# Performance work log

Measured on AMD Instinct MI355X. Metric: run time of the kernel, lower is better.

The kernel has to match this reference:

```python
import jax, jax.numpy as jnp
import numpy as np

B, N, IN_DIM, OUT_DIM, HEADS = 8, 1024, 128, 64, 4

def setup_inputs() -> dict:
    key = jax.random.key(0)
    k1, k2, k3, k4 = jax.random.split(key, 4)
    H = jax.random.normal(k1, (B, N, IN_DIM), dtype=jnp.float32)
    A = jax.random.randint(k2, (B, N, N), 0, 2, dtype=jnp.int32)
    W = jax.random.normal(k3, (IN_DIM, OUT_DIM * HEADS), dtype=jnp.float32) * (1.0 / np.sqrt(IN_DIM))
    a = jax.random.normal(k4, (HEADS, 2 * OUT_DIM), dtype=jnp.float32)
    return {"H": H, "A": A, "W": W, "a": a}

def reference(H, A, W, a):
    Bb, Nn, _ = H.shape
    # Linear projection -> [B, H, N, D]
    Ht = (H @ W).reshape(Bb, Nn, HEADS, OUT_DIM).transpose(0, 2, 1, 3)
    # Split attention vector: e[b,h,n,m] = a_src.Ht[n] + a_dst.Ht[m]
    a_src, a_dst = a[:, :OUT_DIM], a[:, OUT_DIM:]
    e_src = jnp.einsum('bhnd,hd->bhn', Ht, a_src)  # [B,H,N]
    e_dst = jnp.einsum('bhmd,hd->bhm', Ht, a_dst)  # [B,H,N]
    e = e_src[:, :, :, None] + e_dst[:, :, None, :]  # [B,H,N,N]
    e = jax.nn.leaky_relu(e, negative_slope=0.2)
    mask = (A[:, None, :, :] == 0)  # [B,1,N,N]
    e = jnp.where(mask, jnp.float32(-1e9), e)
    alpha = jax.nn.softmax(e, axis=-1)
    H_att = jnp.einsum('bhnm,bhmd->bhnd', alpha, Ht)
    H_out = H_att.transpose(0, 2, 1, 3).reshape(Bb, Nn, HEADS * OUT_DIM)
    return jax.nn.elu(H_out)
```

## Files before the change

kernel.cpp:

```cpp
#include <hip/hip_runtime.h>
#include <hip/hip_bf16.h>
#include <cstdint>
#include <cmath>

#define B_   8
#define N_   1024
#define IND  128
#define D_   64
#define H_   4
#define BH_  (B_*H_)

typedef __attribute__((ext_vector_type(8))) short short8;
typedef __attribute__((ext_vector_type(4))) short shortx4;
typedef __attribute__((ext_vector_type(4))) float f32x4;

__device__ inline short f2bf(float f) {
  __hip_bfloat16 h = __float2bfloat16(f);
  return *reinterpret_cast<short*>(&h);
}

__global__ __launch_bounds__(256) void k_proj(
    const float* __restrict__ H, const float* __restrict__ W,
    const float* __restrict__ a, short* __restrict__ HtT,
    float* __restrict__ esrc, float* __restrict__ edst) {
  __shared__ float hrow[4 * IND];
  const int tid = threadIdx.x;
  const int row0 = blockIdx.x * 4;
  const float* src = H + (size_t)row0 * IND;
  hrow[tid]       = src[tid];
  hrow[tid + 256] = src[tid + 256];
  __syncthreads();

  const int w = tid >> 6;
  const int lane = tid & 63;
  float acc0 = 0.f, acc1 = 0.f, acc2 = 0.f, acc3 = 0.f;
  #pragma unroll 4
  for (int k = 0; k < IND; ++k) {
    float wk = W[k * 256 + tid];
    acc0 = fmaf(hrow[k],           wk, acc0);
    acc1 = fmaf(hrow[IND + k],     wk, acc1);
    acc2 = fmaf(hrow[2 * IND + k], wk, acc2);
    acc3 = fmaf(hrow[3 * IND + k], wk, acc3);
  }
  const float asrc = a[w * 2 * D_ + lane];
  const float adst = a[w * 2 * D_ + D_ + lane];
  float accs[4] = {acc0, acc1, acc2, acc3};

  const int b = row0 >> 10;
  const int n = row0 & (N_ - 1);
  shortx4 hv;
  #pragma unroll
  for (int r = 0; r < 4; ++r) hv[r] = f2bf(accs[r]);
  *(shortx4*)(HtT + ((size_t)((b * H_ + w) * D_ + lane)) * N_ + n) = hv;

  #pragma unroll
  for (int r = 0; r < 4; ++r) {
    float es = accs[r] * asrc;
    float ed = accs[r] * adst;
    #pragma unroll
    for (int off = 32; off >= 1; off >>= 1) {
      es += __shfl_xor(es, off);
      ed += __shfl_xor(ed, off);
    }
    if (lane == 0) {
      size_t eo = (size_t)(b * H_ + w) * N_ + n + r;
      esrc[eo] = es;
      edst[eo] = ed;
    }
  }
}

__global__ __launch_bounds__(256) void k_attn(
    const short* __restrict__ HtT, const float* __restrict__ esrc,
    const float* __restrict__ edst, const int* __restrict__ A,
    float* __restrict__ out) {
  __shared__ float accL[4][16][68];
  __shared__ float MSl[2][4][16];

  const int blk = blockIdx.x;
  const int bh = blk >> 6;
  const int n0 = (blk & 63) * 16;
  const int b = bh >> 2, h = bh & 3;
  const int tid = threadIdx.x, wv = tid >> 6, lane = tid & 63;
  const int r15 = lane & 15, g = lane >> 4;

  const float* edp = edst + (size_t)bh * N_;
  const short* Hp  = HtT + (size_t)bh * D_ * N_;
  const int*   Ap0 = A + (size_t)b * N_ * N_ + (size_t)(n0 + r15) * N_;

  const float es_own = esrc[(size_t)bh * N_ + n0 + r15];

  const int mbase = wv * 256;

  float s[8][8];
  #pragma unroll
  for (int c = 0; c < 8; ++c) {
    const int mg = mbase + c * 32 + g * 8;
    float4 e0 = *(const float4*)(edp + mg);
    float4 e1 = *(const float4*)(edp + mg + 4);
    int4 a0 = *(const int4*)(Ap0 + mg);
    int4 a1 = *(const int4*)(Ap0 + mg + 4);
    float ev[8] = {e0.x, e0.y, e0.z, e0.w, e1.x, e1.y, e1.z, e1.w};
    int   av[8] = {a0.x, a0.y, a0.z, a0.w, a1.x, a1.y, a1.z, a1.w};
    #pragma unroll
    for (int e = 0; e < 8; ++e) {
      float t = es_own + ev[e];
      t = fmaxf(t, 0.2f * t);
      s[c][e] = av[e] ? t : -1e9f;
    }
  }

  float M = -INFINITY;
  #pragma unroll
  for (int c = 0; c < 8; ++c)
    #pragma unroll
    for (int e = 0; e < 8; ++e) M = fmaxf(M, s[c][e]);
  M = fmaxf(M, __shfl_xor(M, 16));
  M = fmaxf(M, __shfl_xor(M, 32));

  f32x4 acc[4] = {};
  float psum = 0.f;
  #pragma unroll
  for (int c = 0; c < 8; ++c) {
    const int mg = mbase + c * 32 + g * 8;
    short8 pa;
    #pragma unroll
    for (int e = 0; e < 8; ++e) {
      float p = __expf(s[c][e] - M);
      psum += p;
      pa[e] = f2bf(p);
    }
    #pragma unroll
    for (int q = 0; q < 4; ++q) {
      short8 bq = *(const short8*)(Hp + (size_t)(q * 16 + r15) * N_ + mg);
      acc[q] = __builtin_amdgcn_mfma_f32_16x16x32_bf16(pa, bq, acc[q], 0, 0, 0);
    }
  }
  psum += __shfl_xor(psum, 16);
  psum += __shfl_xor(psum, 32);

  #pragma unroll
  for (int q = 0; q < 4; ++q)
    #pragma unroll
    for (int j = 0; j < 4; ++j)
      accL[wv][g * 4 + j][q * 16 + r15] = acc[q][j];
  if (g == 0) { MSl[0][wv][r15] = M; MSl[1][wv][r15] = psum; }
  __syncthreads();

  const int row = tid >> 4, d0 = (tid & 15) * 4;
  float Mw[4], Sw[4], Mg = -INFINITY;
  #pragma unroll
  for (int w = 0; w < 4; ++w) {
    Mw[w] = MSl[0][w][row]; Sw[w] = MSl[1][w][row];
    Mg = fmaxf(Mg, Mw[w]);
  }
  float Sg = 0.f;
  float o[4] = {0.f, 0.f, 0.f, 0.f};
  #pragma unroll
  for (int w = 0; w < 4; ++w) {
    float f = __expf(Mw[w] - Mg);
    Sg += Sw[w] * f;
    float4 av = *(const float4*)&accL[w][row][d0];
    o[0] = fmaf(av.x, f, o[0]); o[1] = fmaf(av.y, f, o[1]);
    o[2] = fmaf(av.z, f, o[2]); o[3] = fmaf(av.w, f, o[3]);
  }
  const float inv = 1.f / Sg;
  float4 ov;
  float vx = o[0] * inv; ov.x = vx > 0.f ? vx : expm1f(vx);
  float vy = o[1] * inv; ov.y = vy > 0.f ? vy : expm1f(vy);
  float vz = o[2] * inv; ov.z = vz > 0.f ? vz : expm1f(vz);
  float vw = o[3] * inv; ov.w = vw > 0.f ? vw : expm1f(vw);
  *(float4*)(out + ((size_t)(b * N_ + n0 + row)) * (H_ * D_) + h * D_ + d0) = ov;
}

extern "C" void kernel_launch(void* const* d_in, const int* in_sizes, int n_in,
                              void* d_out, int out_size, void* d_ws, size_t ws_size,
                              hipStream_t stream) {
  const float* H = (const float*)d_in[0];
  const int*   A = (const int*)d_in[1];
  const float* W = (const float*)d_in[2];
  const float* a = (const float*)d_in[3];
  float* out = (float*)d_out;

  short* HtT  = (short*)d_ws;
  float* esrc = (float*)((char*)d_ws + (size_t)BH_ * D_ * N_ * 2);
  float* edst = esrc + (size_t)BH_ * N_;

  k_proj<<<B_ * N_ / 4, 256, 0, stream>>>(H, W, a, HtT, esrc, edst);
  k_attn<<<BH_ * (N_ / 16), 256, 0, stream>>>(HtT, esrc, edst, A, out);
}
```

Baseline: 143.5 us.

## Pack adjacency mask into bitmask and reorder attention blocks for reuse

Adds a pre-pass kernel that compresses the int32 adjacency matrix into 64-bit ballot bitmasks, so the attention kernel reads 1 bit per edge instead of 4 bytes for every head. It also remaps block indices so that blocks sharing a batch and row tile run close together. The goal is to cut the dominant mask memory traffic, at the cost of one extra kernel launch and a full read of A in the pack pass.

```diff
diff --git a/kernel.cpp b/kernel.cpp
--- a/kernel.cpp
+++ b/kernel.cpp
@@ -17,6 +17,20 @@
 __device__ inline short f2bf(float f) {
   __hip_bfloat16 h = __float2bfloat16(f);
   return *reinterpret_cast<short*>(&h);
+}
+
+__global__ __launch_bounds__(256) void k_pack(
+    const int* __restrict__ A, unsigned long long* __restrict__ Abits) {
+  const int tid = threadIdx.x, wv = tid >> 6, lane = tid & 63;
+  const int row = blockIdx.x * 4 + wv;
+  const int* Ar = A + (size_t)row * N_;
+  unsigned long long* Out = Abits + (size_t)row * 16;
+  #pragma unroll
+  for (int c = 0; c < 16; ++c) {
+    int v = Ar[c * 64 + lane];
+    unsigned long long bits = __ballot(v != 0);
+    if (lane == 0) Out[c] = bits;
+  }
 }
 
 __global__ __launch_bounds__(256) void k_proj(
@@ -72,41 +86,41 @@
 
 __global__ __launch_bounds__(256) void k_attn(
     const short* __restrict__ HtT, const float* __restrict__ esrc,
-    const float* __restrict__ edst, const int* __restrict__ A,
+    const float* __restrict__ edst, const unsigned* __restrict__ Abits,
     float* __restrict__ out) {
   __shared__ float accL[4][16][68];
   __shared__ float MSl[2][4][16];
 
   const int blk = blockIdx.x;
-  const int bh = blk >> 6;
-  const int n0 = (blk & 63) * 16;
+  const int x = blk & 7, y = blk >> 3;
+  const int bh = (y & 3) * 8 + x;
+  const int n0 = (y >> 2) * 16;
   const int b = bh >> 2, h = bh & 3;
   const int tid = threadIdx.x, wv = tid >> 6, lane = tid & 63;
   const int r15 = lane & 15, g = lane >> 4;
 
   const float* edp = edst + (size_t)bh * N_;
   const short* Hp  = HtT + (size_t)bh * D_ * N_;
-  const int*   Ap0 = A + (size_t)b * N_ * N_ + (size_t)(n0 + r15) * N_;
+  const unsigned* Abp = Abits + ((size_t)(b * N_ + n0 + r15)) * 32;
 
   const float es_own = esrc[(size_t)bh * N_ + n0 + r15];
+  const int gs = g * 8;
 
   const int mbase = wv * 256;
 
   float s[8][8];
   #pragma unroll
   for (int c = 0; c < 8; ++c) {
-    const int mg = mbase + c * 32 + g * 8;
+    const int mg = mbase + c * 32 + gs;
     float4 e0 = *(const float4*)(edp + mg);
     float4 e1 = *(const float4*)(edp + mg + 4);
-    int4 a0 = *(const int4*)(Ap0 + mg);
-    int4 a1 = *(const int4*)(Ap0 + mg + 4);
+    unsigned ab = Abp[wv * 8 + c] >> gs;
     float ev[8] = {e0.x, e0.y, e0.z, e0.w, e1.x, e1.y, e1.z, e1.w};
-    int   av[8] = {a0.x, a0.y, a0.z, a0.w, a1.x, a1.y, a1.z, a1.w};
     #pragma unroll
     for (int e = 0; e < 8; ++e) {
       float t = es_own + ev[e];
       t = fmaxf(t, 0.2f * t);
-      s[c][e] = av[e] ? t : -1e9f;
+      s[c][e] = ((ab >> e) & 1u) ? t : -1e9f;
     }
   }
 
@@ -122,7 +136,7 @@
   float psum = 0.f;
   #pragma unroll
   for (int c = 0; c < 8; ++c) {
-    const int mg = mbase + c * 32 + g * 8;
+    const int mg = mbase + c * 32 + gs;
     short8 pa;
     #pragma unroll
     for (int e = 0; e < 8; ++e) {
@@ -185,7 +199,11 @@
   short* HtT  = (short*)d_ws;
   float* esrc = (float*)((char*)d_ws + (size_t)BH_ * D_ * N_ * 2);
   float* edst = esrc + (size_t)BH_ * N_;
-
+  unsigned long long* Abits =
+      (unsigned long long*)(edst + (size_t)BH_ * N_);
+
+  k_pack<<<B_ * N_ / 4, 256, 0, stream>>>(A, Abits);
   k_proj<<<B_ * N_ / 4, 256, 0, stream>>>(H, W, a, HtT, esrc, edst);
-  k_attn<<<BH_ * (N_ / 16), 256, 0, stream>>>(HtT, esrc, edst, A, out);
-}
+  k_attn<<<BH_ * (N_ / 16), 256, 0, stream>>>(HtT, esrc, edst,
+                                              (const unsigned*)Abits, out);
+}
```

New measurement: 143.4 us. About the same (-0.1%).
